# Kernel optimization log

Hardware: AMD Instinct MI355X
Metric: run time of the kernel (lower is better)

Reference implementation:

```python
import jax, jax.numpy as jnp
import numpy as np

B, N, C = 2, 2048, 1536
H = 8
D = C // H  # 192, must match M's size


def setup_inputs() -> dict:
    key = jax.random.key(0)
    ks = jax.random.split(key, 5)
    x = jax.random.normal(ks[0], (B, N, C), dtype=jnp.float32)
    # nn.Linear(dim, 3*dim, bias=False): weight shape (3C, C)
    W_qkv = jax.random.normal(ks[1], (3 * C, C), dtype=jnp.float32) * (C ** -0.5)
    # nn.Linear(dim, dim) with bias
    W_proj = jax.random.normal(ks[2], (C, C), dtype=jnp.float32) * (C ** -0.5)
    b_proj = jnp.zeros((C,), dtype=jnp.float32)
    scale = jnp.asarray(D ** -0.5, dtype=jnp.float32)  # learned scalar, init head_dim**-0.5
    M = jnp.eye(D, dtype=jnp.float32)  # learned Mahalanobis metric, init identity
    return {"x": x, "W_qkv": W_qkv, "W_proj": W_proj, "b_proj": b_proj,
            "scale": scale, "M": M}


def reference(x, W_qkv, W_proj, b_proj, scale, M):
    Bv, Nv, Cv = x.shape
    qkv = x @ W_qkv.T                                  # [B,N,3C]
    qkv = qkv.reshape(Bv, Nv, 3, H, D).transpose(2, 0, 3, 1, 4)  # [3,B,H,N,D]
    q, k, v = qkv[0], qkv[1], qkv[2]
    q_M = q @ M                                        # [B,H,N,D]
    k_M = k @ M                                        # [B,H,N,D]
    qMq = jnp.sum(q * q_M, axis=-1, keepdims=True)     # [B,H,N,1]
    kMk = jnp.sum(k * k_M, axis=-1, keepdims=True)     # [B,H,N,1]
    kMk = jnp.swapaxes(kMk, -2, -1)                    # [B,H,1,N]
    qMk = jnp.einsum('bhnd,bhmd->bhnm', q_M, k)        # [B,H,N,N]
    dists = qMq + kMk - 2.0 * qMk                      # Mahalanobis quadratic form
    attn = jax.nn.softmax(-dists * scale, axis=-1)     # [B,H,N,N]
    out = jnp.einsum('bhnm,bhmd->bhnd', attn, v)       # [B,H,N,D]
    out = jnp.swapaxes(out, 1, 2).reshape(Bv, Nv, Cv)  # [B,N,C]
    out = out @ W_proj.T + b_proj
    return (out, attn, M)
```

## Files before the change

### kernel.cpp

```cpp
#include <hip/hip_runtime.h>

typedef _Float16 f16;
typedef __attribute__((ext_vector_type(8))) _Float16 f16x8;
typedef __attribute__((ext_vector_type(4))) float f32x4;

#define LOG2E 1.4426950408889634f
#define MFMA16(a, b, c) __builtin_amdgcn_mfma_f32_16x16x32_f16((a), (b), (c), 0, 0, 0)


__device__ __forceinline__ void gl16(const void* g, void* l) {
    __builtin_amdgcn_global_load_lds(
        (const __attribute__((address_space(1))) unsigned int*)g,
        (__attribute__((address_space(3))) unsigned int*)l, 16, 0, 0);
}

__global__ void k_cvt_all(const float* __restrict__ x, const float* __restrict__ wq,
                          const float* __restrict__ wp, f16* __restrict__ xh,
                          f16* __restrict__ wqh, f16* __restrict__ wph) {
    int i = blockIdx.x * 256 + threadIdx.x;
    const float4* s; short4* d; int off;
    if (i < 1572864) { s = (const float4*)x; d = (short4*)xh; off = i; }
    else if (i < 3342336) { s = (const float4*)wq; d = (short4*)wqh; off = i - 1572864; }
    else { s = (const float4*)wp; d = (short4*)wph; off = i - 3342336; }
    float4 v = s[off];
    union { f16 h[4]; short4 s4; } u;
    u.h[0] = (f16)v.x; u.h[1] = (f16)v.y; u.h[2] = (f16)v.z; u.h[3] = (f16)v.w;
    d[off] = u.s4;
}

__global__ void k_cvtM(const float* __restrict__ M, f16* __restrict__ Mt) {
    int i = blockIdx.x * 256 + threadIdx.x;
    if (i >= 192 * 192) return;
    int d = i / 192, e = i - (i / 192) * 192;
    Mt[d * 192 + e] = (f16)M[e * 192 + d];
}

__global__ __launch_bounds__(256) void k_gemm_qkv(
    const f16* __restrict__ A, const f16* __restrict__ Bw,
    f16* __restrict__ Qh, f16* __restrict__ Kh, f16* __restrict__ Vp)
{
    __shared__ __align__(16) char S[32768];
    const int tid = threadIdx.x, lane = tid & 63, w = tid >> 6;
    const int bid = blockIdx.x;
    const int xcd = bid & 7, cc = bid >> 3;
    const int mb = xcd * 4 + cc / 36, nb = cc - (cc / 36) * 36;
    const int m0 = mb * 128, n0 = nb * 128;
    const int sec = nb >= 24 ? 2 : (nb >= 12 ? 1 : 0);
    const int wm = (w & 1) * 64, wn = (w >> 1) * 64;
    const int L = lane & 15, g = lane >> 4;
    const char* Ab = (const char*)A;
    const char* Bb = (const char*)Bw;

    const char* gA[2]; const char* gB[2]; int ldso[2];
#pragma unroll
    for (int q = 0; q < 2; ++q) {
        int s = w * 128 + q * 64 + lane;
        int swz = ((s & 3) ^ ((s >> 2) & 3)) * 16;
        gA[q] = Ab + (size_t)(m0 + (s >> 2)) * 3072 + swz;
        gB[q] = Bb + (size_t)(n0 + (s >> 2)) * 3072 + swz;
        ldso[q] = w * 2048 + q * 1024;
    }
    const int gx = ((g ^ (L & 3)) << 4);

    f32x4 acc[4][4] = {};
#pragma unroll
    for (int q = 0; q < 2; ++q) {
        gl16(gA[q], S + ldso[q]);
        gl16(gB[q], S + 8192 + ldso[q]);
    }
    int buf = 0;
    for (int kk = 0; kk < 48; ++kk) {
        __syncthreads();
        if (kk < 47) {
            int nb_ = (buf ^ 1) * 16384;
#pragma unroll
            for (int q = 0; q < 2; ++q) {
                gl16(gA[q] + (kk + 1) * 64, S + nb_ + ldso[q]);
                gl16(gB[q] + (kk + 1) * 64, S + nb_ + 8192 + ldso[q]);
            }
        }
        const char* AsB = S + buf * 16384;
        const char* BsB = AsB + 8192;
        f16x8 af[4], bf[4];
#pragma unroll
        for (int i = 0; i < 4; ++i) {
            af[i] = *(const f16x8*)(AsB + (wm + i * 16 + L) * 64 + gx);
            bf[i] = *(const f16x8*)(BsB + (wn + i * 16 + L) * 64 + gx);
        }
        if (sec < 2) {
#pragma unroll
            for (int i = 0; i < 4; ++i)
#pragma unroll
                for (int j = 0; j < 4; ++j)
                    acc[i][j] = MFMA16(bf[j], af[i], acc[i][j]);
        } else {
#pragma unroll
            for (int i = 0; i < 4; ++i)
#pragma unroll
                for (int j = 0; j < 4; ++j)
                    acc[i][j] = MFMA16(af[i], bf[j], acc[i][j]);
        }
        buf ^= 1;
    }

    if (sec == 2) {
#pragma unroll
        for (int i = 0; i < 4; ++i)
#pragma unroll
            for (int j = 0; j < 4; ++j) {
                int rem = n0 + wn + j * 16 + L - 3072;
                int h = rem / 192, d = rem - h * 192;
                int gm = m0 + wm + i * 16 + g * 4;
                int gb = gm >> 11, nn = gm & 2047;
                union { f16 h4[4]; short4 s4; } u;
#pragma unroll
                for (int r = 0; r < 4; ++r) u.h4[r] = (f16)acc[i][j][r];
                int nnp = (nn & ~31) | (((nn >> 2) & 3) << 3) | (((nn >> 4) & 1) << 2) | (nn & 3);
                *(short4*)(Vp + (size_t)((gb * 8 + h) * 192 + d) * 2048 + nnp) = u.s4;
            }
    } else {
        f16* base = sec == 0 ? Qh : Kh;
#pragma unroll
        for (int i = 0; i < 4; ++i) {
            int gm = m0 + wm + i * 16 + L;
            int gb = gm >> 11, nn = gm & 2047;
#pragma unroll
            for (int j = 0; j < 4; ++j) {
                int rem = n0 + wn + j * 16 + g * 4 - sec * 1536;
                int h = rem / 192, d = rem - h * 192;
                union { f16 h4[4]; short4 s4; } u;
#pragma unroll
                for (int r = 0; r < 4; ++r) u.h4[r] = (f16)acc[i][j][r];
                *(short4*)(base + (size_t)((gb * 8 + h) * 2048 + nn) * 192 + d) = u.s4;
            }
        }
    }
}

__global__ __launch_bounds__(256) void k_mgemm(
    const f16* __restrict__ Qh, const f16* __restrict__ Kh,
    const f16* __restrict__ Mt, f16* __restrict__ QMh,
    const float* __restrict__ scale_p, float* __restrict__ qmq, float* __restrict__ kmk)
{
    const int tid = threadIdx.x, lane = tid & 63, w = tid >> 6;
    const int L = lane & 15, g = lane >> 4;
    const int isK = blockIdx.y;
    const f16* src = isK ? Kh : Qh;
    float* rowdot = isK ? kmk : qmq;
    const int row0 = blockIdx.x * 64 + w * 16;
    const int tokrow = row0 + L;
    f16x8 af[6];
#pragma unroll
    for (int ks = 0; ks < 6; ++ks)
        af[ks] = *(const f16x8*)((const char*)src + (size_t)tokrow * 384 + ks * 64 + g * 16);
    f32x4 acc[12] = {};
#pragma unroll
    for (int ct = 0; ct < 12; ++ct)
#pragma unroll
        for (int ks = 0; ks < 6; ++ks) {
            f16x8 bf = *(const f16x8*)((const char*)Mt + (ct * 16 + L) * 384 + ks * 64 + g * 16);
            acc[ct] = MFMA16(bf, af[ks], acc[ct]);
        }
    if (!isK) {
#pragma unroll
        for (int ct = 0; ct < 12; ++ct) {
            union { f16 h4[4]; short4 s4; } u;
#pragma unroll
            for (int r = 0; r < 4; ++r) u.h4[r] = (f16)acc[ct][r];
            *(short4*)(QMh + (size_t)tokrow * 192 + ct * 16 + g * 4) = u.s4;
        }
    }
    float s = 0.f;
#pragma unroll
    for (int ct = 0; ct < 12; ++ct) {
        union { short4 s4; f16 h[4]; } kv;
        kv.s4 = *(const short4*)(src + (size_t)tokrow * 192 + ct * 16 + g * 4);
#pragma unroll
        for (int r = 0; r < 4; ++r) s += acc[ct][r] * (float)kv.h[r];
    }
    s += __shfl_xor(s, 16); s += __shfl_xor(s, 32);
    if (lane < 16) rowdot[row0 + lane] = s * scale_p[0] * LOG2E;
}

__global__ __launch_bounds__(256) void k_attn(
    const f16* __restrict__ QMh, const f16* __restrict__ Kh,
    const f16* __restrict__ Vp, const float* __restrict__ kmk,
    const float* __restrict__ qmq, const float* __restrict__ scale_p,
    float* __restrict__ attn, f16* __restrict__ ctx)
{
    __shared__ __align__(16) char KsB[2][12288];
    __shared__ __align__(16) char VsB[2][15360];
    const int tid = threadIdx.x, lane = tid & 63, w = tid >> 6;
    const int L = lane & 15, g = lane >> 4;
    const int bx = blockIdx.x;
    const int bh = (bx & 7) * 2 + (bx >> 8);
    const int qb = (bx >> 3) & 31;
    const int row0 = qb * 64 + w * 16;
    const float a2 = 2.f * scale_p[0] * LOG2E;

    const char* qbase = (const char*)QMh + (size_t)(bh * 2048 + row0) * 384;
    f16x8 qf[6];
#pragma unroll
    for (int ks = 0; ks < 6; ++ks)
        qf[ks] = *(const f16x8*)(qbase + L * 384 + ks * 64 + g * 16);
    const char* Kb = (const char*)Kh + (size_t)bh * 2048 * 384;
    const char* Vb = (const char*)Vp + (size_t)bh * 192 * 4096;
    const float* kmkrow = kmk + bh * 2048;
    const float Crow = qmq[bh * 2048 + row0 + L];

    int ksrc[3], kdst[3], vsrc[3], vdst[3];
#pragma unroll
    for (int i = 0; i < 3; ++i) {
        int s = tid + 256 * i;
        int r = s / 24, c16 = s - r * 24;
        ksrc[i] = r * 384 + c16 * 16;
        kdst[i] = r * 384 + (((c16 & ~7) | ((c16 & 7) ^ (r & 7))) << 4);
        vsrc[i] = (s >> 2) * 4096 + (s & 3) * 16;
        vdst[i] = (s >> 2) * 80 + (s & 3) * 16;
    }
    int kslot[6];
#pragma unroll
    for (int ks = 0; ks < 6; ++ks) {
        int slot = ks * 4 + g;
        kslot[ks] = (((slot & ~7) | ((slot & 7) ^ (L & 7))) << 4);
    }

    int4 stk[3], stv[3];
#pragma unroll
    for (int i = 0; i < 3; ++i) {
        stk[i] = *(const int4*)(Kb + ksrc[i]);
        stv[i] = *(const int4*)(Vb + vsrc[i]);
    }
    f32x4 cacc[12] = {};
    float lacc = 0.f;
    float m_run = -3.0e38f, sc = 0.f;
    float* arow = attn + (size_t)(bh * 2048 + row0 + L) * 2048;

    for (int c = 0; c < 64; ++c) {
        char* Kl = KsB[c & 1];
        char* Vl = VsB[c & 1];
#pragma unroll
        for (int i = 0; i < 3; ++i) {
            *(int4*)(Kl + kdst[i]) = stk[i];
            *(int4*)(Vl + vdst[i]) = stv[i];
        }
        if (c < 63) {
#pragma unroll
            for (int i = 0; i < 3; ++i) {
                stk[i] = *(const int4*)(Kb + (size_t)(c + 1) * 12288 + ksrc[i]);
                stv[i] = *(const int4*)(Vb + (size_t)(c + 1) * 64 + vsrc[i]);
            }
        }
        __syncthreads();
        f32x4 a0 = {}, a1 = {};
#pragma unroll
        for (int ks = 0; ks < 6; ++ks) {
            f16x8 kf0 = *(const f16x8*)(Kl + L * 384 + kslot[ks]);
            f16x8 kf1 = *(const f16x8*)(Kl + (16 + L) * 384 + kslot[ks]);
            a0 = MFMA16(kf0, qf[ks], a0);
            a1 = MFMA16(kf1, qf[ks], a1);
        }
        float4 km0 = *(const float4*)(kmkrow + c * 32 + g * 4);
        float4 km1 = *(const float4*)(kmkrow + c * 32 + 16 + g * 4);
        float e8[8];
        e8[0] = a2 * a0[0] - km0.x - Crow;
        e8[1] = a2 * a0[1] - km0.y - Crow;
        e8[2] = a2 * a0[2] - km0.z - Crow;
        e8[3] = a2 * a0[3] - km0.w - Crow;
        e8[4] = a2 * a1[0] - km1.x - Crow;
        e8[5] = a2 * a1[1] - km1.y - Crow;
        e8[6] = a2 * a1[2] - km1.z - Crow;
        e8[7] = a2 * a1[3] - km1.w - Crow;
        float mx = fmaxf(fmaxf(fmaxf(e8[0], e8[1]), fmaxf(e8[2], e8[3])),
                         fmaxf(fmaxf(e8[4], e8[5]), fmaxf(e8[6], e8[7])));
        mx = fmaxf(mx, __shfl_xor(mx, 16));
        mx = fmaxf(mx, __shfl_xor(mx, 32));
        if (__any(mx > m_run + 4.f)) {
            float mnew = fmaxf(m_run, mx);
            float fr = __builtin_amdgcn_exp2f(m_run - mnew);
            lacc *= fr;
            float frc[4];
#pragma unroll
            for (int r = 0; r < 4; ++r) frc[r] = __shfl(fr, g * 4 + r);
#pragma unroll
            for (int dt = 0; dt < 12; ++dt)
#pragma unroll
                for (int r = 0; r < 4; ++r) cacc[dt][r] *= frc[r];
            m_run = mnew;
            sc = __builtin_amdgcn_exp2f(-m_run);
        }
        float p[8], ps[8];
#pragma unroll
        for (int j = 0; j < 8; ++j) {
            p[j] = __builtin_amdgcn_exp2f(e8[j]);
            ps[j] = p[j] * sc;
        }
        *(float4*)(arow + c * 32 + g * 4)      = make_float4(p[0], p[1], p[2], p[3]);
        *(float4*)(arow + c * 32 + 16 + g * 4) = make_float4(p[4], p[5], p[6], p[7]);
        lacc += ((ps[0] + ps[1]) + (ps[2] + ps[3])) + ((ps[4] + ps[5]) + (ps[6] + ps[7]));
        f16x8 pa;
        pa[0] = (f16)ps[0]; pa[1] = (f16)ps[1]; pa[2] = (f16)ps[2]; pa[3] = (f16)ps[3];
        pa[4] = (f16)ps[4]; pa[5] = (f16)ps[5]; pa[6] = (f16)ps[6]; pa[7] = (f16)ps[7];
#pragma unroll
        for (int dt = 0; dt < 12; ++dt) {
            f16x8 vf = *(const f16x8*)(Vl + (dt * 16 + L) * 80 + g * 16);
            cacc[dt] = MFMA16(pa, vf, cacc[dt]);
        }
    }
    lacc += __shfl_xor(lacc, 16);
    lacc += __shfl_xor(lacc, 32);
    const float fnorm = __builtin_amdgcn_exp2f(-m_run) / lacc;
    float linv_r[4];
#pragma unroll
    for (int r = 0; r < 4; ++r) linv_r[r] = 1.f / __shfl(lacc, g * 4 + r);

#pragma unroll 4
    for (int c = 0; c < 64; ++c) {
        f32x4 v0 = *(const f32x4*)(arow + c * 32 + g * 4);
        f32x4 v1 = *(const f32x4*)(arow + c * 32 + 16 + g * 4);
        v0 *= fnorm;
        v1 *= fnorm;
        __builtin_nontemporal_store(v0, (f32x4*)(arow + c * 32 + g * 4));
        __builtin_nontemporal_store(v1, (f32x4*)(arow + c * 32 + 16 + g * 4));
    }

    __syncthreads();
    char* scr = (char*)KsB + w * 6144;
#pragma unroll
    for (int dt = 0; dt < 12; ++dt)
#pragma unroll
        for (int r = 0; r < 4; ++r)
            *(f16*)(scr + (g * 4 + r) * 384 + (dt * 16 + L) * 2)
                = (f16)(cacc[dt][r] * linv_r[r]);
    const int b = bh >> 3, h = bh & 7;
#pragma unroll
    for (int t = 0; t < 6; ++t) {
        int chunk = t * 64 + lane;
        int tok = chunk / 24, c16 = chunk - tok * 24;
        int4 v = *(const int4*)(scr + tok * 384 + c16 * 16);
        *(int4*)((char*)ctx + ((size_t)(b * 2048 + row0 + tok) * 1536 + h * 192) * 2 + c16 * 16) = v;
    }
}

__global__ __launch_bounds__(256) void k_proj(
    const f16* __restrict__ A, const f16* __restrict__ Bw,
    const float* __restrict__ bias, float* __restrict__ out)
{
    __shared__ __align__(16) char S[32768];
    const int tid = threadIdx.x, lane = tid & 63, w = tid >> 6;
    const int bid = blockIdx.x;
    const int xcd = bid & 7, cc = bid >> 3;
    const int mb = xcd * 4 + cc / 12, nbk = cc - (cc / 12) * 12;
    const int m0 = mb * 128, n0 = nbk * 128;
    const int wm = (w & 1) * 64, wn = (w >> 1) * 64;
    const int L = lane & 15, g = lane >> 4;
    const char* Ab = (const char*)A;
    const char* Bb = (const char*)Bw;

    const char* gA[2]; const char* gB[2]; int ldso[2];
#pragma unroll
    for (int q = 0; q < 2; ++q) {
        int s = w * 128 + q * 64 + lane;
        int swz = ((s & 3) ^ ((s >> 2) & 3)) * 16;
        gA[q] = Ab + (size_t)(m0 + (s >> 2)) * 3072 + swz;
        gB[q] = Bb + (size_t)(n0 + (s >> 2)) * 3072 + swz;
        ldso[q] = w * 2048 + q * 1024;
    }
    const int gx = ((g ^ (L & 3)) << 4);

    f32x4 acc[4][4] = {};
#pragma unroll
    for (int q = 0; q < 2; ++q) {
        gl16(gA[q], S + ldso[q]);
        gl16(gB[q], S + 8192 + ldso[q]);
    }
    int buf = 0;
    for (int kk = 0; kk < 48; ++kk) {
        __syncthreads();
        if (kk < 47) {
            int nb_ = (buf ^ 1) * 16384;
#pragma unroll
            for (int q = 0; q < 2; ++q) {
                gl16(gA[q] + (kk + 1) * 64, S + nb_ + ldso[q]);
                gl16(gB[q] + (kk + 1) * 64, S + nb_ + 8192 + ldso[q]);
            }
        }
        const char* AsB = S + buf * 16384;
        const char* BsB = AsB + 8192;
        f16x8 af[4], bf[4];
#pragma unroll
        for (int i = 0; i < 4; ++i) {
            af[i] = *(const f16x8*)(AsB + (wm + i * 16 + L) * 64 + gx);
            bf[i] = *(const f16x8*)(BsB + (wn + i * 16 + L) * 64 + gx);
        }
#pragma unroll
        for (int i = 0; i < 4; ++i)
#pragma unroll
            for (int j = 0; j < 4; ++j)
                acc[i][j] = MFMA16(bf[j], af[i], acc[i][j]);
        buf ^= 1;
    }
#pragma unroll
    for (int i = 0; i < 4; ++i) {
        int token = m0 + wm + i * 16 + L;
#pragma unroll
        for (int j = 0; j < 4; ++j) {
            int gnb = n0 + wn + j * 16 + g * 4;
            float4 bv = *(const float4*)(bias + gnb);
            float4 v = make_float4(acc[i][j][0] + bv.x, acc[i][j][1] + bv.y,
                                   acc[i][j][2] + bv.z, acc[i][j][3] + bv.w);
            *(float4*)(out + (size_t)token * 1536 + gnb) = v;
        }
    }
}

extern "C" void kernel_launch(void* const* d_in, const int* in_sizes, int n_in,
                              void* d_out, int out_size, void* d_ws, size_t ws_size,
                              hipStream_t stream)
{
    const float* x     = (const float*)d_in[0];
    const float* Wqkv  = (const float*)d_in[1];
    const float* Wproj = (const float*)d_in[2];
    const float* bproj = (const float*)d_in[3];
    const float* scale = (const float*)d_in[4];
    const float* M     = (const float*)d_in[5];
    float* out  = (float*)d_out;
    float* attn = out + 6291456;

    char* p = (char*)d_ws;
    f16* x_h     = (f16*)p;  p += 12582912;
    f16* Wqkv_h  = (f16*)p;  p += 14155776;
    f16* Wproj_h = (f16*)p;  p += 4718592;
    f16* Mt_h    = (f16*)p;  p += 73728;
    f16* Qh      = (f16*)p;  p += 12582912;
    f16* Kh      = (f16*)p;  p += 12582912;
    f16* Vp      = (f16*)p;  p += 12582912;
    f16* QMh     = (f16*)p;  p += 12582912;
    float* qmq   = (float*)p; p += 131072;
    float* kmk   = (float*)p; p += 131072;
    f16* ctx     = (f16*)p;  p += 12582912;

    k_cvt_all<<<15360, 256, 0, stream>>>(x, Wqkv, Wproj, x_h, Wqkv_h, Wproj_h);
    k_cvtM<<<144, 256, 0, stream>>>(M, Mt_h);
    k_gemm_qkv<<<1152, 256, 0, stream>>>(x_h, Wqkv_h, Qh, Kh, Vp);
    k_mgemm<<<dim3(512, 2), 256, 0, stream>>>(Qh, Kh, Mt_h, QMh, scale, qmq, kmk);
    k_attn<<<512, 256, 0, stream>>>(QMh, Kh, Vp, kmk, qmq, scale, attn, ctx);
    k_proj<<<384, 256, 0, stream>>>(ctx, Wproj_h, bproj, out);
    hipMemcpyAsync(out + 73400320, M, 36864 * 4, hipMemcpyDeviceToDevice, stream);
}
```

Before: 448.4 us.

## Defer attention-row normalization into projection kernel as extra blocks

The per-row rescaling of the attention matrix moves out of the attention kernel. The attention kernel now only stores a per-row factor, exp2(-m)/l, into a new workspace buffer. A combined tail kernel then runs the output projection GEMM blocks alongside 4096 extra blocks that rescale the stored attention rows in place. The aim is to overlap the memory-bound rescale pass with the compute-bound projection and to shorten the attention kernel's tail. In exchange the attention matrix is re-read from memory instead of possibly from cache right after it was written.

Result: faster. 415.6 us (-7.3%).

```diff
diff --git a/kernel.cpp b/kernel.cpp
--- a/kernel.cpp
+++ b/kernel.cpp
@@ -186,7 +186,7 @@
     const f16* __restrict__ QMh, const f16* __restrict__ Kh,
     const f16* __restrict__ Vp, const float* __restrict__ kmk,
     const float* __restrict__ qmq, const float* __restrict__ scale_p,
-    float* __restrict__ attn, f16* __restrict__ ctx)
+    float* __restrict__ attn, f16* __restrict__ ctx, float* __restrict__ lrow)
 {
     __shared__ __align__(16) char KsB[2][12288];
     __shared__ __align__(16) char VsB[2][15360];
@@ -309,20 +309,10 @@
     }
     lacc += __shfl_xor(lacc, 16);
     lacc += __shfl_xor(lacc, 32);
-    const float fnorm = __builtin_amdgcn_exp2f(-m_run) / lacc;
+    if (g == 0) lrow[bh * 2048 + row0 + L] = __builtin_amdgcn_exp2f(-m_run) / lacc;
     float linv_r[4];
 #pragma unroll
     for (int r = 0; r < 4; ++r) linv_r[r] = 1.f / __shfl(lacc, g * 4 + r);
-
-#pragma unroll 4
-    for (int c = 0; c < 64; ++c) {
-        f32x4 v0 = *(const f32x4*)(arow + c * 32 + g * 4);
-        f32x4 v1 = *(const f32x4*)(arow + c * 32 + 16 + g * 4);
-        v0 *= fnorm;
-        v1 *= fnorm;
-        __builtin_nontemporal_store(v0, (f32x4*)(arow + c * 32 + g * 4));
-        __builtin_nontemporal_store(v1, (f32x4*)(arow + c * 32 + 16 + g * 4));
-    }
 
     __syncthreads();
     char* scr = (char*)KsB + w * 6144;
@@ -342,12 +332,28 @@
     }
 }
 
-__global__ __launch_bounds__(256) void k_proj(
+__global__ __launch_bounds__(256) void k_tail(
     const f16* __restrict__ A, const f16* __restrict__ Bw,
-    const float* __restrict__ bias, float* __restrict__ out)
+    const float* __restrict__ bias, float* __restrict__ out,
+    float* __restrict__ attn, const float* __restrict__ lrow)
 {
+    const int tid = threadIdx.x;
+    if (blockIdx.x >= 384) {
+        const int row = (blockIdx.x - 384) * 8 + (tid >> 5);
+        const int t = tid & 31;
+        const float f = lrow[row];
+        float* base = attn + (size_t)row * 2048;
+#pragma unroll
+        for (int i = 0; i < 16; ++i) {
+            f32x4* p = (f32x4*)(base + i * 128) + t;
+            f32x4 v = *p;
+            v *= f;
+            __builtin_nontemporal_store(v, p);
+        }
+        return;
+    }
     __shared__ __align__(16) char S[32768];
-    const int tid = threadIdx.x, lane = tid & 63, w = tid >> 6;
+    const int lane = tid & 63, w = tid >> 6;
     const int bid = blockIdx.x;
     const int xcd = bid & 7, cc = bid >> 3;
     const int mb = xcd * 4 + cc / 12, nbk = cc - (cc / 12) * 12;
@@ -438,13 +444,14 @@
     f16* QMh     = (f16*)p;  p += 12582912;
     float* qmq   = (float*)p; p += 131072;
     float* kmk   = (float*)p; p += 131072;
+    float* lrow  = (float*)p; p += 131072;
     f16* ctx     = (f16*)p;  p += 12582912;
 
     k_cvt_all<<<15360, 256, 0, stream>>>(x, Wqkv, Wproj, x_h, Wqkv_h, Wproj_h);
     k_cvtM<<<144, 256, 0, stream>>>(M, Mt_h);
     k_gemm_qkv<<<1152, 256, 0, stream>>>(x_h, Wqkv_h, Qh, Kh, Vp);
     k_mgemm<<<dim3(512, 2), 256, 0, stream>>>(Qh, Kh, Mt_h, QMh, scale, qmq, kmk);
-    k_attn<<<512, 256, 0, stream>>>(QMh, Kh, Vp, kmk, qmq, scale, attn, ctx);
-    k_proj<<<384, 256, 0, stream>>>(ctx, Wproj_h, bproj, out);
+    k_attn<<<512, 256, 0, stream>>>(QMh, Kh, Vp, kmk, qmq, scale, attn, ctx, lrow);
+    k_tail<<<4480, 256, 0, stream>>>(ctx, Wproj_h, bproj, out, attn, lrow);
     hipMemcpyAsync(out + 73400320, M, 36864 * 4, hipMemcpyDeviceToDevice, stream);
 }
```
